# Optimization experiments

Measured on AMD Instinct MI355X. Metric: run time of the kernel, lower is better.

The kernel has to match this reference:

```python
import jax, jax.numpy as jnp
import numpy as np

# irreps_in = 64x0e + 32x1o + 16x2e ; output of FCTP = 64x0e
MULS = (64, 32, 16)
LS = (0, 1, 2)
IRR_DIM = sum(m * (2 * l + 1) for m, l in zip(MULS, LS))  # 240
HID = 64   # hidden_fea_len
Z = 64     # z_fea_len
N = 50000
# e3nn path normalization ('element', normalization='component'):
# each l x l -> 0e path weight = sqrt(ir_out.dim / sum_paths(mul1*mul2)) = 1/sqrt(64^2+32^2+16^2)
PATH_NORM = 1.0 / np.sqrt(sum(m * m for m in MULS))


def _split(t):
    # slice flat irrep vector into per-irrep [N, mul, 2l+1] blocks
    blocks, i = [], 0
    for m, l in zip(MULS, LS):
        d = 2 * l + 1
        blocks.append(t[:, i:i + m * d].reshape(-1, m, d))
        i += m * d
    return blocks


def _fctp(t, W0, W1, W2):
    # FullyConnectedTensorProduct(irr, irr, '64x0e'):
    # for each l, CG w3j(l,l,0)[m,m'] = delta_{mm'} / sqrt(2l+1),
    # out[n,k] = sum_l pw_l * sum_{u,v} W_l[u,v,k] * <x_l[n,u,:], x_l[n,v,:]> / sqrt(2l+1)
    out = 0.0
    for x, W, l in zip(_split(t), (W0, W1, W2), LS):
        d = 2 * l + 1
        dot = jnp.einsum('num,nvm->nuv', x, x) * (PATH_NORM / np.sqrt(d))
        out = out + jnp.einsum('nuv,uvk->nk', dot, W)
    return out


def _mlp(h, A1, b1, A2, b2, A3, b3):
    h = jax.nn.silu(h @ A1.T + b1)
    h = jax.nn.silu(h @ A2.T + b2)
    return h @ A3.T + b3


def setup_inputs() -> dict:
    key = jax.random.key(0)
    ks = jax.random.split(key, 8)
    return {
        'tensor_in': jax.random.normal(ks[0], (N, IRR_DIM), jnp.float32),
        # FCTP weights (e3nn init: standard normal; normalization lives in PATH_NORM)
        'W0': jax.random.normal(ks[1], (64, 64, HID), jnp.float32),
        'W1': jax.random.normal(ks[2], (32, 32, HID), jnp.float32),
        'W2': jax.random.normal(ks[3], (16, 16, HID), jnp.float32),
        # nn.Linear params (y = x @ A.T + b)
        'A1': jax.random.normal(ks[4], (HID, HID), jnp.float32) / np.sqrt(HID),
        'b1': jnp.zeros((HID,), jnp.float32),
        'A2': jax.random.normal(ks[5], (Z, HID), jnp.float32) / np.sqrt(HID),
        'b2': jnp.zeros((Z,), jnp.float32),
        'A3': jax.random.normal(ks[6], (Z, Z), jnp.float32) / np.sqrt(Z),
        'b3': jnp.zeros((Z,), jnp.float32),
    }


def reference(tensor_in, W0, W1, W2, A1, b1, A2, b2, A3, b3):
    def fwd(t):
        return _mlp(_fctp(t, W0, W1, W2), A1, b1, A2, b2, A3, b3)

    # x = MLP(FCTP(t, t)); y = d(sum(x))/dt  (autograd.grad with ones grad_outputs)
    x, vjp_fn = jax.vjp(fwd, tensor_in)
    y = vjp_fn(jnp.ones_like(x))[0]
    return (x, y)
```

## Files before the change

### kernel.cpp

```cpp
#include <hip/hip_runtime.h>
#include <math.h>
#include <utility>


typedef short bf8 __attribute__((ext_vector_type(8)));
typedef float f4 __attribute__((ext_vector_type(4)));

constexpr int IRR = 240;

constexpr int NP = 2880;

struct PTab { short u[NP]; short v[NP]; signed char l[NP]; };
constexpr PTab build_ptab() {
    PTab t{}; int p = 0;
    for (int u = 0; u < 64; u++) for (int v = u; v < 64; v++) { t.u[p]=(short)u; t.v[p]=(short)v; t.l[p]=0; p++; }
    while (p < 2112) { t.l[p] = -1; p++; }
    for (int u = 0; u < 32; u++) for (int v = u; v < 32; v++) { t.u[p]=(short)u; t.v[p]=(short)v; t.l[p]=1; p++; }
    while (p < 2688) { t.l[p] = -1; p++; }
    for (int u = 0; u < 16; u++) for (int v = u; v < 16; v++) { t.u[p]=(short)u; t.v[p]=(short)v; t.l[p]=2; p++; }
    while (p < NP)   { t.l[p] = -1; p++; }
    return t;
}
constexpr PTab PT = build_ptab();

constexpr size_t B_WTF = 0;
constexpr size_t B_WB  = (size_t)64 * NP * 2;
constexpr size_t B_A1T = B_WB + (size_t)5376 * 64 * 2;
constexpr size_t B_A2T = B_A1T + 16384;
constexpr size_t B_A3T = B_A2T + 16384;
constexpr size_t B_DG2 = B_A3T + 16384;
constexpr size_t B_H   = B_DG2 + 256;

__device__ __forceinline__ unsigned short f2bf(float x) {
    unsigned int u = __float_as_uint(x);
    return (unsigned short)((u + 0x7fffu + ((u >> 16) & 1u)) >> 16);
}
__device__ __forceinline__ unsigned pack2(float a, float b) {
    unsigned ua = __float_as_uint(a) + 0x8000u;
    unsigned ub = __float_as_uint(b) + 0x8000u;
    return __builtin_amdgcn_perm(ub, ua, 0x07060302u);
}

__global__ void prep_kernel(const float* __restrict__ W0, const float* __restrict__ W1,
                            const float* __restrict__ W2, const float* __restrict__ A1,
                            const float* __restrict__ A2, const float* __restrict__ A3,
                            unsigned short* __restrict__ wtf, unsigned short* __restrict__ wb,
                            float* __restrict__ a1t, float* __restrict__ a2t,
                            float* __restrict__ a3t, float* __restrict__ dg2)
{
    int idx = blockIdx.x * blockDim.x + threadIdx.x;
    const double c0 = 1.0 / sqrt(5376.0);
    const double cl_[3] = { c0, c0 / sqrt(3.0), c0 / sqrt(5.0) };
    if (idx < 64 * NP) {
        int c = idx / NP, p = idx - c * NP;
        unsigned short val = 0;
        int l = -1, local = 0, mul = 0;
        if (p < 2112)      { local = p;        if (local < 2080) { l = 0; mul = 64; } }
        else if (p < 2688) { local = p - 2112; if (local < 528)  { l = 1; mul = 32; } }
        else               { local = p - 2688; if (local < 136)  { l = 2; mul = 16; } }
        if (l >= 0) {
            int u = 0;
            while ((u + 1) * mul - (u + 1) * u / 2 <= local) u++;
            int v = u + (local - (u * mul - u * (u - 1) / 2));
            const float* W = (l == 0) ? W0 : (l == 1) ? W1 : W2;
            float wv = W[(u * mul + v) * 64 + c];
            if (u != v) wv += W[(v * mul + u) * 64 + c];
            val = f2bf((float)(cl_[l] * wv));
        }
        wtf[(size_t)c * NP + p] = val;
        return;
    }
    idx -= 64 * NP;
    if (idx < 5376 * 64) {
        int pair = idx >> 6, c = idx & 63;
        int l, w, v, mul;
        if (pair < 4096)      { l = 0; mul = 64; w = pair >> 6;          v = pair & 63; }
        else if (pair < 5120) { l = 1; mul = 32; w = (pair - 4096) >> 5; v = (pair - 4096) & 31; }
        else                  { l = 2; mul = 16; w = (pair - 5120) >> 4; v = (pair - 5120) & 15; }
        const float* W = (l == 0) ? W0 : (l == 1) ? W1 : W2;
        float val;
        if (v == w) val = (float)(2.0 * cl_[l]) * W[(w * mul + w) * 64 + c];
        else        val = (float)cl_[l] * (W[(w * mul + v) * 64 + c] + W[(v * mul + w) * 64 + c]);
        wb[(size_t)pair * 64 + c] = f2bf(val);
        return;
    }
    idx -= 5376 * 64;
    if (idx < 3 * 4096) {
        int m = idx >> 12, e = idx & 4095;
        int j = e >> 6, k = e & 63;
        const float* A = (m == 0) ? A1 : (m == 1) ? A2 : A3;
        float* dst     = (m == 0) ? a1t : (m == 1) ? a2t : a3t;
        dst[j * 64 + k] = A[k * 64 + j];
        return;
    }
    idx -= 3 * 4096;
    if (idx < 64) {
        float s = 0.f;
        for (int k = 0; k < 64; k++) s += A3[k * 64 + idx];
        dg2[idx] = s;
    }
}

template <int P, int NX>
__device__ __forceinline__ float pval(const float (&x)[NX]) {
    constexpr int l = PT.l[P];
    if constexpr (l < 0) {
        return 0.f;
    } else if constexpr (l == 0) {
        return x[PT.u[P]] * x[PT.v[P]];
    } else if constexpr (l == 1) {
        constexpr int u = 3 * PT.u[P], v = 3 * PT.v[P];
        return x[u] * x[v] + x[u + 1] * x[v + 1] + x[u + 2] * x[v + 2];
    } else {
        constexpr int u = 5 * PT.u[P], v = 5 * PT.v[P];
        return x[u] * x[v] + x[u + 1] * x[v + 1] + x[u + 2] * x[v + 2]
             + x[u + 3] * x[v + 3] + x[u + 4] * x[v + 4];
    }
}

template <int CH, int O, int NX>
__device__ __forceinline__ void p_octet(const float (&xr)[NX],
        unsigned short (&Pb)[64][64], int lane)
{
    uint4 w;
    w.x = pack2(pval<CH * 64 + O * 8 + 0, NX>(xr), pval<CH * 64 + O * 8 + 1, NX>(xr));
    w.y = pack2(pval<CH * 64 + O * 8 + 2, NX>(xr), pval<CH * 64 + O * 8 + 3, NX>(xr));
    w.z = pack2(pval<CH * 64 + O * 8 + 4, NX>(xr), pval<CH * 64 + O * 8 + 5, NX>(xr));
    w.w = pack2(pval<CH * 64 + O * 8 + 6, NX>(xr), pval<CH * 64 + O * 8 + 7, NX>(xr));
    *(uint4*)&Pb[lane][(O ^ (lane & 7)) * 8] = w;
}

template <int CH, int NX, int... Os>
__device__ __forceinline__ void p_octets(std::integer_sequence<int, Os...>,
        const float (&xr)[NX], unsigned short (&Pb)[64][64], int lane)
{
    (p_octet<CH, Os, NX>(xr, Pb, lane), ...);
}

template <int CH, int NX>
__device__ __forceinline__ void fwd_chunk(const float (&xr)[NX],
        unsigned short (&Pb)[64][64], const unsigned short* __restrict__ wtf,
        f4 (&acc)[4][4], int lane, int l15, int quad)
{
    p_octets<CH, NX>(std::make_integer_sequence<int, 8>{}, xr, Pb, lane);
    asm volatile("s_waitcnt lgkmcnt(0)" ::: "memory");
    bf8 a[4][2];
    #pragma unroll
    for (int rt = 0; rt < 4; ++rt) {
        int row = 16 * rt + l15;
        #pragma unroll
        for (int ks = 0; ks < 2; ++ks)
            a[rt][ks] = *(const bf8*)&Pb[row][((ks * 4 + quad) ^ (row & 7)) * 8];
    }
    #pragma unroll
    for (int ct = 0; ct < 4; ++ct) {
        #pragma unroll
        for (int ks = 0; ks < 2; ++ks) {
            bf8 b = *(const bf8*)(wtf + (size_t)(16 * ct + l15) * NP + CH * 64 + ks * 32 + quad * 8);
            #pragma unroll
            for (int rt = 0; rt < 4; ++rt)
                acc[rt][ct] = __builtin_amdgcn_mfma_f32_16x16x32_bf16(a[rt][ks], b, acc[rt][ct], 0, 0, 0);
        }
    }
    asm volatile("" ::: "memory");
}

template <int B, int NX, int... Is>
__device__ __forceinline__ void fwd_run(std::integer_sequence<int, Is...>,
        const float (&xr)[NX], unsigned short (&Pb)[64][64],
        const unsigned short* __restrict__ wtf, f4 (&acc)[4][4],
        int lane, int l15, int quad)
{
    (fwd_chunk<B + Is, NX>(xr, Pb, wtf, acc, lane, l15, quad), ...);
}

__global__ __launch_bounds__(256) void fctp_fwd4(const float* __restrict__ tin,
        const unsigned short* __restrict__ wtf, float* __restrict__ h, int n)
{
    __shared__ unsigned short Pb[4][64][64];
    const int tid = threadIdx.x;
    const int wv = tid >> 6;
    const int lane = tid & 63;
    const int l15 = lane & 15, quad = lane >> 4;
    const int s0 = blockIdx.x * 64;
    const int s = s0 + lane;
    const int sld = (s < n) ? s : (n - 1);
    const float* xrow = tin + (size_t)sld * IRR;
    f4 acc[4][4];
    #pragma unroll
    for (int rt = 0; rt < 4; ++rt)
        #pragma unroll
        for (int ct = 0; ct < 4; ++ct) acc[rt][ct] = (f4){0.f, 0.f, 0.f, 0.f};

    if (wv == 0) {
        float x0[64];
        #pragma unroll
        for (int q = 0; q < 16; ++q) *(float4*)&x0[4 * q] = *(const float4*)(xrow + 4 * q);
        fwd_run<0>(std::make_integer_sequence<int, 17>{}, x0, Pb[0], wtf, acc, lane, l15, quad);
    } else if (wv == 1) {
        float x0[64];
        #pragma unroll
        for (int q = 0; q < 16; ++q) *(float4*)&x0[4 * q] = *(const float4*)(xrow + 4 * q);
        fwd_run<17>(std::make_integer_sequence<int, 16>{}, x0, Pb[1], wtf, acc, lane, l15, quad);
    } else if (wv == 2) {
        float x1[96];
        #pragma unroll
        for (int q = 0; q < 24; ++q) *(float4*)&x1[4 * q] = *(const float4*)(xrow + 64 + 4 * q);
        fwd_run<33>(std::make_integer_sequence<int, 9>{}, x1, Pb[2], wtf, acc, lane, l15, quad);
    } else {
        float x2[80];
        #pragma unroll
        for (int q = 0; q < 20; ++q) *(float4*)&x2[4 * q] = *(const float4*)(xrow + 160 + 4 * q);
        fwd_run<42>(std::make_integer_sequence<int, 3>{}, x2, Pb[3], wtf, acc, lane, l15, quad);
    }

    float* red = (float*)Pb;
    #pragma unroll
    for (int rt = 0; rt < 4; ++rt) {
        __syncthreads();
        #pragma unroll
        for (int ct = 0; ct < 4; ++ct) {
            float4 v = make_float4(acc[rt][ct][0], acc[rt][ct][1], acc[rt][ct][2], acc[rt][ct][3]);
            *(float4*)&red[(size_t)(wv * 64 + lane) * 20 + ct * 4] = v;
        }
        __syncthreads();
        float4 sum = make_float4(0.f, 0.f, 0.f, 0.f);
        #pragma unroll
        for (int w = 0; w < 4; ++w) {
            float4 v = *(const float4*)&red[(size_t)(w * 64 + lane) * 20 + wv * 4];
            sum.x += v.x; sum.y += v.y; sum.z += v.z; sum.w += v.w;
        }
        #pragma unroll
        for (int r = 0; r < 4; ++r) {
            int row = s0 + 16 * rt + 4 * quad + r;
            if (row < n) h[(size_t)row * 64 + 16 * wv + l15] = (&sum.x)[r];
        }
    }
}

__device__ __forceinline__ void bwd_mm(int ch, const unsigned short* __restrict__ wb,
        const bf8 (&bh)[4][2], float (*dPb)[68],
        int lane, int l15, int quad)
{
    f4 dp[4][4];
    #pragma unroll
    for (int rt = 0; rt < 4; ++rt)
        #pragma unroll
        for (int ct = 0; ct < 4; ++ct) dp[rt][ct] = (f4){0.f, 0.f, 0.f, 0.f};
    #pragma unroll
    for (int rt = 0; rt < 4; ++rt) {
        #pragma unroll
        for (int ks = 0; ks < 2; ++ks) {
            bf8 a = *(const bf8*)(wb + (size_t)(ch * 64 + 16 * rt + l15) * 64 + ks * 32 + quad * 8);
            #pragma unroll
            for (int ct = 0; ct < 4; ++ct)
                dp[rt][ct] = __builtin_amdgcn_mfma_f32_16x16x32_bf16(a, bh[ct][ks], dp[rt][ct], 0, 0, 0);
        }
    }
    #pragma unroll
    for (int rt = 0; rt < 4; ++rt)
        #pragma unroll
        for (int ct = 0; ct < 4; ++ct) {
            float4 v = make_float4(dp[rt][ct][0], dp[rt][ct][1], dp[rt][ct][2], dp[rt][ct][3]);
            *(float4*)&dPb[16 * ct + l15][16 * rt + 4 * quad] = v;
        }
    asm volatile("s_waitcnt lgkmcnt(0)" ::: "memory");
}

__global__ __launch_bounds__(64) void fctp_bwd_g(const float* __restrict__ tin,
        const unsigned short* __restrict__ wb, const float* __restrict__ dh,
        float* __restrict__ y, int n)
{
    __shared__ __align__(16) unsigned char smem[64 * 68 * 4];
    float (*dPb)[68] = (float (*)[68])smem;
    unsigned short (*dhb)[64] = (unsigned short (*)[64])smem;

    const int lane = threadIdx.x;
    const int l15 = lane & 15, quad = lane >> 4;
    const int s0 = blockIdx.x * 64;
    const int s = s0 + lane;
    const int sld = (s < n) ? s : (n - 1);
    const bool act = s < n;
    {
        const float* dhp = dh + (size_t)sld * 64;
        #pragma unroll
        for (int o = 0; o < 8; ++o) {
            float4 f0 = *(const float4*)(dhp + 8 * o);
            float4 f1 = *(const float4*)(dhp + 8 * o + 4);
            uint4 w = make_uint4(pack2(f0.x, f0.y), pack2(f0.z, f0.w),
                                 pack2(f1.x, f1.y), pack2(f1.z, f1.w));
            *(uint4*)&dhb[lane][(o ^ (lane & 7)) * 8] = w;
        }
    }
    asm volatile("s_waitcnt lgkmcnt(0)" ::: "memory");
    bf8 bh[4][2];
    #pragma unroll
    for (int ct = 0; ct < 4; ++ct) {
        int row = 16 * ct + l15;
        #pragma unroll
        for (int ks = 0; ks < 2; ++ks)
            bh[ct][ks] = *(const bf8*)&dhb[row][((ks * 4 + quad) ^ (row & 7)) * 8];
    }
    asm volatile("" ::: "memory");
    const float* xrow = tin + (size_t)sld * IRR;
    float* yrow = y + (size_t)sld * IRR;

    const int g = blockIdx.y;
    if (g < 4) {
        float x0[64];
        #pragma unroll
        for (int q = 0; q < 16; ++q) *(float4*)&x0[4 * q] = *(const float4*)(xrow + 4 * q);
        const int cbase = g * 16;
        for (int i = 0; i < 16; ++i) {
            const int ch = cbase + i;
            bwd_mm(ch, wb, bh, dPb, lane, l15, quad);
            float a0 = 0.f, a1 = 0.f, a2 = 0.f, a3 = 0.f;
            #pragma unroll
            for (int p = 0; p < 64; p += 4) {
                float4 d = *(const float4*)&dPb[lane][p];
                a0 += d.x * x0[p];     a1 += d.y * x0[p + 1];
                a2 += d.z * x0[p + 2]; a3 += d.w * x0[p + 3];
            }
            if (act) yrow[ch] = (a0 + a1) + (a2 + a3);
        }
    } else if (g < 6) {
        float x1[96];
        #pragma unroll
        for (int q = 0; q < 24; ++q) *(float4*)&x1[4 * q] = *(const float4*)(xrow + 64 + 4 * q);
        const int cbase = (g - 4) * 8;
        for (int i = 0; i < 8; ++i) {
            const int c1 = cbase + i;
            bwd_mm(64 + c1, wb, bh, dPb, lane, l15, quad);
            float r[2][3] = {{0.f, 0.f, 0.f}, {0.f, 0.f, 0.f}};
            #pragma unroll
            for (int v = 0; v < 32; v += 4) {
                float4 dA = *(const float4*)&dPb[lane][v];
                float4 dB = *(const float4*)&dPb[lane][32 + v];
                #pragma unroll
                for (int vv = 0; vv < 4; ++vv) {
                    float da = (&dA.x)[vv], db = (&dB.x)[vv];
                    #pragma unroll
                    for (int m = 0; m < 3; ++m) {
                        r[0][m] += da * x1[3 * (v + vv) + m];
                        r[1][m] += db * x1[3 * (v + vv) + m];
                    }
                }
            }
            if (act) {
                #pragma unroll
                for (int wi = 0; wi < 2; ++wi)
                    #pragma unroll
                    for (int m = 0; m < 3; ++m)
                        yrow[64 + (2 * c1 + wi) * 3 + m] = r[wi][m];
            }
        }
    } else {
        float x2[80];
        #pragma unroll
        for (int q = 0; q < 20; ++q) *(float4*)&x2[4 * q] = *(const float4*)(xrow + 160 + 4 * q);
        for (int c2 = 0; c2 < 4; ++c2) {
            bwd_mm(80 + c2, wb, bh, dPb, lane, l15, quad);
            float r[4][5] = {};
            #pragma unroll
            for (int t = 0; t < 4; ++t) {
                #pragma unroll
                for (int v = 0; v < 16; v += 4) {
                    float4 d = *(const float4*)&dPb[lane][t * 16 + v];
                    #pragma unroll
                    for (int vv = 0; vv < 4; ++vv)
                        #pragma unroll
                        for (int m = 0; m < 5; ++m)
                            r[t][m] += (&d.x)[vv] * x2[5 * (v + vv) + m];
                }
            }
            if (act) {
                #pragma unroll
                for (int t = 0; t < 4; ++t)
                    #pragma unroll
                    for (int m = 0; m < 5; ++m)
                        yrow[160 + (4 * c2 + t) * 5 + m] = r[t][m];
            }
        }
    }
}

__global__ __launch_bounds__(256) void mlp4(
    const float* __restrict__ h, const float* __restrict__ A1,
    const float* __restrict__ A2, const float* __restrict__ a1t,
    const float* __restrict__ a2t, const float* __restrict__ a3t,
    const float* __restrict__ b1, const float* __restrict__ b2,
    const float* __restrict__ b3, const float* __restrict__ dg2,
    float* __restrict__ xout, float* __restrict__ dhout, int n)
{
    __shared__ float sact[64][65];
    const int tid  = threadIdx.x;
    const int lane = tid & 63;
    const int ch0  = __builtin_amdgcn_readfirstlane((tid >> 6) * 16);
    const int s    = blockIdx.x * 64 + lane;
    const bool valid = s < n;
    const int sld  = valid ? s : (n - 1);

    {
        const float* hp = h + (size_t)sld * 64 + ch0;
        #pragma unroll
        for (int q = 0; q < 4; ++q) {
            float4 v = *(const float4*)(hp + 4 * q);
            sact[lane][ch0 + 4 * q + 0] = v.x;
            sact[lane][ch0 + 4 * q + 1] = v.y;
            sact[lane][ch0 + 4 * q + 2] = v.z;
            sact[lane][ch0 + 4 * q + 3] = v.w;
        }
    }
    __syncthreads();

    float acc[16], z1[16], z2[16];

    #pragma unroll
    for (int k = 0; k < 16; ++k) acc[k] = b1[ch0 + k];
    #pragma unroll 4
    for (int j = 0; j < 64; ++j) {
        float aj = sact[lane][j];
        const float* r = a1t + j * 64 + ch0;
        #pragma unroll
        for (int k = 0; k < 16; ++k) acc[k] += aj * r[k];
    }
    __syncthreads();
    #pragma unroll
    for (int k = 0; k < 16; ++k) {
        float z = acc[k]; z1[k] = z;
        float sg = 1.f / (1.f + __expf(-z));
        sact[lane][ch0 + k] = z * sg;
    }
    __syncthreads();

    #pragma unroll
    for (int k = 0; k < 16; ++k) acc[k] = b2[ch0 + k];
    #pragma unroll 4
    for (int j = 0; j < 64; ++j) {
        float aj = sact[lane][j];
        const float* r = a2t + j * 64 + ch0;
        #pragma unroll
        for (int k = 0; k < 16; ++k) acc[k] += aj * r[k];
    }
    __syncthreads();
    #pragma unroll
    for (int k = 0; k < 16; ++k) {
        float z = acc[k]; z2[k] = z;
        float sg = 1.f / (1.f + __expf(-z));
        sact[lane][ch0 + k] = z * sg;
    }
    __syncthreads();

    #pragma unroll
    for (int k = 0; k < 16; ++k) acc[k] = b3[ch0 + k];
    #pragma unroll 4
    for (int j = 0; j < 64; ++j) {
        float aj = sact[lane][j];
        const float* r = a3t + j * 64 + ch0;
        #pragma unroll
        for (int k = 0; k < 16; ++k) acc[k] += aj * r[k];
    }
    if (valid) {
        float4* xo = (float4*)(xout + (size_t)s * 64 + ch0);
        #pragma unroll
        for (int q = 0; q < 4; ++q)
            xo[q] = make_float4(acc[4 * q], acc[4 * q + 1], acc[4 * q + 2], acc[4 * q + 3]);
    }

    __syncthreads();
    #pragma unroll
    for (int k = 0; k < 16; ++k) {
        float z = z2[k];
        float sg = 1.f / (1.f + __expf(-z));
        sact[lane][ch0 + k] = dg2[ch0 + k] * sg * (1.f + z * (1.f - sg));
    }
    __syncthreads();

    #pragma unroll
    for (int k = 0; k < 16; ++k) acc[k] = 0.f;
    #pragma unroll 4
    for (int kk = 0; kk < 64; ++kk) {
        float d = sact[lane][kk];
        const float* r = A2 + kk * 64 + ch0;
        #pragma unroll
        for (int k = 0; k < 16; ++k) acc[k] += d * r[k];
    }
    __syncthreads();
    #pragma unroll
    for (int k = 0; k < 16; ++k) {
        float z = z1[k];
        float sg = 1.f / (1.f + __expf(-z));
        sact[lane][ch0 + k] = acc[k] * sg * (1.f + z * (1.f - sg));
    }
    __syncthreads();

    #pragma unroll
    for (int k = 0; k < 16; ++k) acc[k] = 0.f;
    #pragma unroll 4
    for (int j = 0; j < 64; ++j) {
        float d = sact[lane][j];
        const float* r = A1 + j * 64 + ch0;
        #pragma unroll
        for (int k = 0; k < 16; ++k) acc[k] += d * r[k];
    }
    if (valid) {
        float4* dho = (float4*)(dhout + (size_t)s * 64 + ch0);
        #pragma unroll
        for (int q = 0; q < 4; ++q)
            dho[q] = make_float4(acc[4 * q], acc[4 * q + 1], acc[4 * q + 2], acc[4 * q + 3]);
    }
}

extern "C" void kernel_launch(void* const* d_in, const int* in_sizes, int n_in,
                              void* d_out, int out_size, void* d_ws, size_t ws_size,
                              hipStream_t stream)
{
    const float* tin = (const float*)d_in[0];
    const float* W0  = (const float*)d_in[1];
    const float* W1  = (const float*)d_in[2];
    const float* W2  = (const float*)d_in[3];
    const float* A1  = (const float*)d_in[4];
    const float* b1  = (const float*)d_in[5];
    const float* A2  = (const float*)d_in[6];
    const float* b2  = (const float*)d_in[7];
    const float* A3  = (const float*)d_in[8];
    const float* b3  = (const float*)d_in[9];
    float* out = (float*)d_out;
    char* ws   = (char*)d_ws;
    const int n = in_sizes[0] / IRR;

    unsigned short* wtf = (unsigned short*)(ws + B_WTF);
    unsigned short* wb  = (unsigned short*)(ws + B_WB);
    float* a1t  = (float*)(ws + B_A1T);
    float* a2t  = (float*)(ws + B_A2T);
    float* a3t  = (float*)(ws + B_A3T);
    float* dg2  = (float*)(ws + B_DG2);
    float* h    = (float*)(ws + B_H);
    float* dh   = h + (size_t)n * 64;
    float* xout = out;
    float* yout = out + (size_t)n * 64;

    const int total_prep = 64 * NP + 5376 * 64 + 3 * 4096 + 64;
    prep_kernel<<<(total_prep + 255) / 256, 256, 0, stream>>>(W0, W1, W2, A1, A2, A3,
                                                              wtf, wb, a1t, a2t, a3t, dg2);
    const int nb64 = (n + 63) / 64;
    fctp_fwd4<<<nb64, 256, 0, stream>>>(tin, wtf, h, n);
    mlp4<<<nb64, 256, 0, stream>>>(h, A1, A2, a1t, a2t, a3t,
                                   b1, b2, b3, dg2, xout, dh, n);
    fctp_bwd_g<<<dim3(nb64, 7), 64, 0, stream>>>(tin, wb, dh, yout, n);
}
```

Baseline: 386.4 us.

## Fuse l=0 backward MFMA output directly with x contraction in registers

For the l=0 channel groups, the backward matmul result is no longer written to the shared dP buffer and re-read per lane. Instead, each MFMA accumulator tile is multiplied against x values arranged in the matching MFMA layout, then reduced across quads with shuffles. Results for four channels are gathered and written with one float4 store. This removes LDS round-trips per channel, at the cost of extra shuffles, more registers, and full unrolling of the channel loop.

```diff
diff --git a/kernel.cpp b/kernel.cpp
--- a/kernel.cpp
+++ b/kernel.cpp
@@ -307,21 +307,52 @@
 
     const int g = blockIdx.y;
     if (g < 4) {
-        float x0[64];
-        #pragma unroll
-        for (int q = 0; q < 16; ++q) *(float4*)&x0[4 * q] = *(const float4*)(xrow + 4 * q);
+        #pragma unroll
+        for (int q = 0; q < 16; ++q)
+            *(float4*)&dPb[lane][4 * q] = *(const float4*)(xrow + 4 * q);
+        asm volatile("s_waitcnt lgkmcnt(0)" ::: "memory");
+        float xr[64];
+        #pragma unroll
+        for (int ct = 0; ct < 4; ++ct)
+            #pragma unroll
+            for (int rt = 0; rt < 4; ++rt)
+                *(float4*)&xr[ct * 16 + rt * 4] =
+                    *(const float4*)&dPb[16 * ct + l15][16 * rt + 4 * quad];
+        asm volatile("" ::: "memory");
+
         const int cbase = g * 16;
+        float res[4];
+        #pragma unroll
         for (int i = 0; i < 16; ++i) {
             const int ch = cbase + i;
-            bwd_mm(ch, wb, bh, dPb, lane, l15, quad);
-            float a0 = 0.f, a1 = 0.f, a2 = 0.f, a3 = 0.f;
+            float p0 = 0.f, p1 = 0.f, p2 = 0.f, p3 = 0.f;
             #pragma unroll
-            for (int p = 0; p < 64; p += 4) {
-                float4 d = *(const float4*)&dPb[lane][p];
-                a0 += d.x * x0[p];     a1 += d.y * x0[p + 1];
-                a2 += d.z * x0[p + 2]; a3 += d.w * x0[p + 3];
+            for (int rt = 0; rt < 4; ++rt) {
+                f4 dpR[4];
+                #pragma unroll
+                for (int ct = 0; ct < 4; ++ct) dpR[ct] = (f4){0.f, 0.f, 0.f, 0.f};
+                #pragma unroll
+                for (int ks = 0; ks < 2; ++ks) {
+                    bf8 a = *(const bf8*)(wb + (size_t)(ch * 64 + 16 * rt + l15) * 64 + ks * 32 + quad * 8);
+                    #pragma unroll
+                    for (int ct = 0; ct < 4; ++ct)
+                        dpR[ct] = __builtin_amdgcn_mfma_f32_16x16x32_bf16(a, bh[ct][ks], dpR[ct], 0, 0, 0);
+                }
+                #pragma unroll
+                for (int r = 0; r < 4; ++r) {
+                    p0 += dpR[0][r] * xr[ 0 + rt * 4 + r];
+                    p1 += dpR[1][r] * xr[16 + rt * 4 + r];
+                    p2 += dpR[2][r] * xr[32 + rt * 4 + r];
+                    p3 += dpR[3][r] * xr[48 + rt * 4 + r];
+                }
             }
-            if (act) yrow[ch] = (a0 + a1) + (a2 + a3);
+            p0 += __shfl_xor(p0, 16); p0 += __shfl_xor(p0, 32);
+            p1 += __shfl_xor(p1, 16); p1 += __shfl_xor(p1, 32);
+            p2 += __shfl_xor(p2, 16); p2 += __shfl_xor(p2, 32);
+            p3 += __shfl_xor(p3, 16); p3 += __shfl_xor(p3, 32);
+            res[i & 3] = (quad == 0) ? p0 : (quad == 1) ? p1 : (quad == 2) ? p2 : p3;
+            if ((i & 3) == 3 && act)
+                *(float4*)&yrow[ch - 3] = make_float4(res[0], res[1], res[2], res[3]);
         }
     } else if (g < 6) {
         float x1[96];
```

New measurement: 408.4 us. 5.7% more time.
